# Performance work log

Hardware: AMD Instinct MI355X
Metric: run time of the kernel (lower is better)

## Reference

```python
import jax, jax.numpy as jnp
import numpy as np

LEAKY_ALPHA = 0.2  # tf.nn.leaky_relu default

B, S, E = 16, 4096, 768
H, A = 4, 128  # segments_amount (heads), attention_dimension


def setup_inputs() -> dict:
    key = jax.random.key(0)
    k0, k1, k2 = jax.random.split(key, 3)
    x = jax.random.normal(k0, (B, S, E), dtype=jnp.float32)
    # Per-head MLP params, Glorot-ish scaling
    W1 = jax.random.normal(k1, (H, E, A), dtype=jnp.float32) * (1.0 / np.sqrt(E))
    b1 = jnp.zeros((H, A), dtype=jnp.float32)
    W2 = jax.random.normal(k2, (H, A, E), dtype=jnp.float32) * (1.0 / np.sqrt(A))
    b2 = jnp.zeros((H, E), dtype=jnp.float32)
    return {"x": x, "W1": W1, "b1": b1, "W2": W2, "b2": b2}


def reference(x, W1, b1, W2, b2):
    # Batched over heads h: Dense->LeakyReLU->Dense
    h = jnp.einsum('bse,hea->bhsa', x, W1) + b1[None, :, None, :]
    h = jnp.where(h >= 0, h, LEAKY_ALPHA * h)
    logits = jnp.einsum('bhsa,hae->bhse', h, W2) + b2[None, :, None, :]
    # Softmax over sequence axis (axis=1 in original per-head [B,S,E])
    weights = jax.nn.softmax(logits, axis=2)  # [B,H,S,E]
    # Attention-weighted sum over sequence -> [B,H,E]
    segment_embeddings = jnp.einsum('bse,bhse->bhe', x, weights)
    return segment_embeddings
```

## Files before the change

### kernel.cpp

```cpp
#include <hip/hip_runtime.h>
#include <hip/hip_bf16.h>

#define B_ 16
#define S_ 4096
#define E_ 768
#define H_ 4
#define A_ 128

constexpr float ALPHA = 0.2f;
constexpr float LOG2E = 1.44269504088896340736f;

typedef __attribute__((ext_vector_type(4))) float f32x4;
typedef __attribute__((ext_vector_type(8))) short bf16x8;

__device__ __forceinline__ unsigned short f2bf(float f) {
    union { float f; unsigned int u; } v;
    v.f = f;
    unsigned int u = v.u;
    unsigned int r = (u + 0x7FFFu + ((u >> 16) & 1u)) >> 16;
    return (unsigned short)r;
}

__device__ __forceinline__ unsigned int pk2bf(float lo, float hi) {
    __hip_bfloat162 h2 = __float22bfloat162_rn(make_float2(lo, hi));
    union { __hip_bfloat162 h; unsigned int u; } c;
    c.h = h2;
    return c.u;
}

__global__ __launch_bounds__(256) void k_prep1(const float* __restrict__ w1,
                                               unsigned short* __restrict__ w1t) {
    __shared__ unsigned short t[64 * 65];
    int bid = blockIdx.x;
    int ta = bid & 1;
    int te = (bid >> 1) % 12;
    int h  = bid / 24;
    const float* src = w1 + (size_t)h * E_ * A_;
    unsigned short* dst = w1t + (size_t)h * A_ * E_;
    int tid = threadIdx.x;
#pragma unroll
    for (int it = 0; it < 16; ++it) {
        int idx = it * 256 + tid;
        int r = idx >> 6, c = idx & 63;
        t[r * 65 + c] = f2bf(src[(size_t)(te * 64 + r) * A_ + ta * 64 + c]);
    }
    __syncthreads();
#pragma unroll
    for (int it = 0; it < 16; ++it) {
        int idx = it * 256 + tid;
        int a = idx >> 6, e = idx & 63;
        dst[(size_t)(ta * 64 + a) * E_ + te * 64 + e] = t[e * 65 + a];
    }
}

__global__ __launch_bounds__(256) void k_prep2(const float* __restrict__ w2,
                                               unsigned short* __restrict__ w2t) {
    __shared__ unsigned short t[64 * 65];
    int bid = blockIdx.x;
    int te = bid % 12;
    int ta = (bid / 12) & 1;
    int h  = bid / 24;
    const float* src = w2 + (size_t)h * A_ * E_;
    unsigned short* dst = w2t + (size_t)h * E_ * A_;
    int tid = threadIdx.x;
#pragma unroll
    for (int it = 0; it < 16; ++it) {
        int idx = it * 256 + tid;
        int r = idx >> 6, c = idx & 63;
        t[r * 65 + c] = f2bf(src[(size_t)(ta * 64 + r) * E_ + te * 64 + c] * LOG2E);
    }
    __syncthreads();
#pragma unroll
    for (int it = 0; it < 16; ++it) {
        int idx = it * 256 + tid;
        int e = idx >> 6, a = idx & 63;
        dst[(size_t)(te * 64 + e) * A_ + ta * 64 + a] = t[a * 65 + e];
    }
}

__global__ __launch_bounds__(512, 4) void k_stage1(
    const float* __restrict__ x, const unsigned short* __restrict__ w1t,
    const float* __restrict__ b1, unsigned short* __restrict__ hm) {

    int bid = blockIdx.x;
    int wid = (bid & 7) * 256 + (bid >> 3);
    const int h  = wid & 3;
    const int st = (wid >> 2) & 31;
    const int b  = wid >> 7;
    const int s0 = st * 128;

    const int tid = threadIdx.x;
    const int wv = tid >> 6, lane = tid & 63;
    const int lr = lane & 15, lg = lane >> 4;
    const int sw = wv & 1, aw = wv >> 1;

    __shared__ unsigned short bufA[128 * 64];
    __shared__ unsigned short bufB[128 * 64];

    const int ar = tid >> 2;
    const int ac = tid & 3;
    const float* xp = x + ((size_t)b * S_ + s0 + ar) * E_ + ac * 16;
    const unsigned short* wp = w1t + ((size_t)h * A_ + ar) * E_ + ac * 8;

    f32x4 acc[4][2];
#pragma unroll
    for (int i = 0; i < 4; ++i)
#pragma unroll
        for (int j = 0; j < 2; ++j) acc[i][j] = (f32x4)0.0f;

    f32x4 xreg[4];
    bf16x8 wreg[2];
#pragma unroll
    for (int l = 0; l < 4; ++l) xreg[l] = *(const f32x4*)(xp + l * 4);
#pragma unroll
    for (int l = 0; l < 2; ++l) wreg[l] = *(const bf16x8*)(wp + l * 32);

#pragma unroll 1
    for (int ks = 0; ks < 12; ++ks) {
        if (ks) __syncthreads();
#pragma unroll
        for (int l = 0; l < 4; ++l) {
            uint2 p;
            p.x = pk2bf(xreg[l][0], xreg[l][1]);
            p.y = pk2bf(xreg[l][2], xreg[l][3]);
            int byte = (ar * 128 + (ac * 4 + l) * 8) ^ ((ar & 7) << 4);
            *(uint2*)((char*)bufA + byte) = p;
        }
#pragma unroll
        for (int l = 0; l < 2; ++l) {
            int byte = (ar * 128 + (ac + l * 4) * 16) ^ ((ar & 7) << 4);
            *(bf16x8*)((char*)bufB + byte) = wreg[l];
        }
        __syncthreads();
        if (ks < 11) {
            const float* xq = xp + (ks + 1) * 64;
#pragma unroll
            for (int l = 0; l < 4; ++l) xreg[l] = *(const f32x4*)(xq + l * 4);
            const unsigned short* wq = wp + (ks + 1) * 64;
#pragma unroll
            for (int l = 0; l < 2; ++l) wreg[l] = *(const bf16x8*)(wq + l * 32);
        }
#pragma unroll
        for (int kk = 0; kk < 2; ++kk) {
            bf16x8 xf[4], wf[2];
#pragma unroll
            for (int sf = 0; sf < 4; ++sf) {
                int r = sw * 64 + sf * 16 + lr;
                xf[sf] = *(const bf16x8*)((char*)bufA + ((r * 128 + kk * 64 + lg * 16) ^ ((r & 7) << 4)));
            }
#pragma unroll
            for (int nf = 0; nf < 2; ++nf) {
                int r = aw * 32 + nf * 16 + lr;
                wf[nf] = *(const bf16x8*)((char*)bufB + ((r * 128 + kk * 64 + lg * 16) ^ ((r & 7) << 4)));
            }
#pragma unroll
            for (int sf = 0; sf < 4; ++sf)
#pragma unroll
                for (int nf = 0; nf < 2; ++nf)
                    acc[sf][nf] = __builtin_amdgcn_mfma_f32_16x16x32_bf16(
                        wf[nf], xf[sf], acc[sf][nf], 0, 0, 0);
        }
    }

    const size_t hb = ((size_t)(b * H_ + h) * S_ + s0 + sw * 64) * A_ + aw * 32;
#pragma unroll
    for (int nf = 0; nf < 2; ++nf) {
        f32x4 bv = *(const f32x4*)(b1 + h * A_ + aw * 32 + nf * 16 + lg * 4);
#pragma unroll
        for (int sf = 0; sf < 4; ++sf) {
            f32x4 v = acc[sf][nf] + bv;
#pragma unroll
            for (int j = 0; j < 4; ++j) v[j] = v[j] >= 0.0f ? v[j] : ALPHA * v[j];
            uint2 p;
            p.x = pk2bf(v[0], v[1]);
            p.y = pk2bf(v[2], v[3]);
            *(uint2*)(hm + hb + (size_t)(sf * 16 + lr) * A_ + nf * 16 + lg * 4) = p;
        }
    }
}

__global__ __launch_bounds__(256, 4) void k_stage2(
    const float* __restrict__ x, const unsigned short* __restrict__ hm,
    const unsigned short* __restrict__ w2t,
    float* __restrict__ part_z, float* __restrict__ part_o) {

    int bid = blockIdx.x;
    int wid = (bid & 7) * 256 + (bid >> 3);
    const int h  = wid & 3;
    const int sc = (wid >> 2) & 31;
    const int b  = wid >> 7;
    const int s0 = sc * 128;

    const int tid = threadIdx.x;
    const int wv = tid >> 6, lane = tid & 63;
    const int lr = lane & 15, lg = lane >> 4;

    __shared__ unsigned short hmt[128 * 128];

    {
        const unsigned short* hp = hm + ((size_t)(b * H_ + h) * S_ + s0) * A_;
        int r = tid >> 1;
        int c = tid & 1;
#pragma unroll
        for (int l = 0; l < 8; ++l) {
            int ch = c * 8 + l;
            bf16x8 v = *(const bf16x8*)(hp + (size_t)r * A_ + ch * 8);
            int byte = (r * 256 + ch * 16) ^ ((r & 7) << 4);
            *(bf16x8*)((char*)hmt + byte) = v;
        }
    }
    __syncthreads();

    const float* xb = x + ((size_t)b * S_ + s0) * E_;
    const unsigned short* w2h = w2t + (size_t)h * E_ * A_;
    const size_t pbase = (size_t)(b * H_ + h) * E_ * 32 + sc;

#pragma unroll 1
    for (int et = 0; et < 6; ++et) {
        const int e0 = et * 128 + wv * 32;
        bf16x8 w2f[2][4];
#pragma unroll
        for (int nf = 0; nf < 2; ++nf) {
            const unsigned short* q = w2h + (size_t)(e0 + nf * 16 + lr) * A_ + lg * 8;
#pragma unroll
            for (int k4 = 0; k4 < 4; ++k4) w2f[nf][k4] = *(const bf16x8*)(q + k4 * 32);
        }
        f32x4 zz[2], oo[2];
#pragma unroll
        for (int nf = 0; nf < 2; ++nf) { zz[nf] = (f32x4)0.0f; oo[nf] = (f32x4)0.0f; }

#pragma unroll 2
        for (int itr = 0; itr < 8; ++itr) {
            int srow = itr * 16 + lr;
            bf16x8 hf[4];
#pragma unroll
            for (int k4 = 0; k4 < 4; ++k4)
                hf[k4] = *(const bf16x8*)((char*)hmt +
                          ((srow * 256 + (k4 * 32 + lg * 8) * 2) ^ ((srow & 7) << 4)));
            f32x4 lac[2];
            lac[0] = (f32x4)0.0f; lac[1] = (f32x4)0.0f;
#pragma unroll
            for (int k4 = 0; k4 < 4; ++k4) {
                lac[0] = __builtin_amdgcn_mfma_f32_16x16x32_bf16(w2f[0][k4], hf[k4], lac[0], 0, 0, 0);
                lac[1] = __builtin_amdgcn_mfma_f32_16x16x32_bf16(w2f[1][k4], hf[k4], lac[1], 0, 0, 0);
            }
#pragma unroll
            for (int nf = 0; nf < 2; ++nf) {
                const float* xq = xb + (size_t)srow * E_ + e0 + nf * 16 + lg * 4;
                f32x4 xv = *(const f32x4*)xq;
                f32x4 pv;
#pragma unroll
                for (int j = 0; j < 4; ++j) pv[j] = exp2f(lac[nf][j]);
                zz[nf] += pv;
                oo[nf] += pv * xv;
            }
        }
#pragma unroll
        for (int nf = 0; nf < 2; ++nf)
#pragma unroll
            for (int j = 0; j < 4; ++j) {
                float zv = zz[nf][j], ov = oo[nf][j];
#pragma unroll
                for (int msk = 1; msk < 16; msk <<= 1) {
                    zv += __shfl_xor(zv, msk);
                    ov += __shfl_xor(ov, msk);
                }
                if (lr == 0) {
                    int e = e0 + nf * 16 + lg * 4 + j;
                    part_z[pbase + (size_t)e * 32] = zv;
                    part_o[pbase + (size_t)e * 32] = ov;
                }
            }
    }
}

__global__ __launch_bounds__(256) void k_merge(const float* __restrict__ part_z,
                                               const float* __restrict__ part_o,
                                               float* __restrict__ out) {
    int idx = blockIdx.x * 256 + threadIdx.x;
    if (idx >= B_ * H_ * E_) return;
    const float* pz = part_z + (size_t)idx * 32;
    const float* po = part_o + (size_t)idx * 32;
    float z = 0.f, o = 0.f;
#pragma unroll
    for (int q = 0; q < 8; ++q) {
        f32x4 a = *(const f32x4*)(pz + q * 4);
        f32x4 c = *(const f32x4*)(po + q * 4);
        z += (a[0] + a[1]) + (a[2] + a[3]);
        o += (c[0] + c[1]) + (c[2] + c[3]);
    }
    out[idx] = o / z;
}

extern "C" void kernel_launch(void* const* d_in, const int* in_sizes, int n_in,
                              void* d_out, int out_size, void* d_ws, size_t ws_size,
                              hipStream_t stream) {
    const float* x  = (const float*)d_in[0];
    const float* w1 = (const float*)d_in[1];
    const float* b1 = (const float*)d_in[2];
    const float* w2 = (const float*)d_in[3];
    float* out = (float*)d_out;

    char* ws = (char*)d_ws;
    unsigned short* hmw    = (unsigned short*)ws;
    unsigned short* w1t    = (unsigned short*)(ws + 67108864);
    unsigned short* w2t    = (unsigned short*)(ws + 67895296);
    float*          part_z = (float*)(ws + 68681728);
    float*          part_o = (float*)(ws + 74973184);

    k_prep1 <<<dim3(96),   256, 0, stream>>>(w1, w1t);
    k_prep2 <<<dim3(96),   256, 0, stream>>>(w2, w2t);
    k_stage1<<<dim3(2048), 512, 0, stream>>>(x, w1t, b1, hmw);
    k_stage2<<<dim3(2048), 256, 0, stream>>>(x, hmw, w2t, part_z, part_o);
    k_merge <<<dim3(192),  256, 0, stream>>>(part_z, part_o, out);
}
```

Before: 547.1 us.

## Load stage-1 MFMA operands directly from global memory, dropping LDS staging

The stage-1 GEMM no longer stages x and W1 tiles through shared memory with barriers. Each wave now loads its MFMA fragments straight from global memory into registers and converts x to bf16 in-register. Loads are double-buffered by hand across k-steps, and the wave tiling changes from 2x4 to 4x2. This removes LDS writes, LDS reads and __syncthreads. The cost is that data is no longer shared across waves, so global/L2 traffic rises and the loads are less coalesced (16 rows, 32-byte chunks per lane).

```diff
diff --git a/kernel.cpp b/kernel.cpp
--- a/kernel.cpp
+++ b/kernel.cpp
@@ -26,6 +26,15 @@
     union { __hip_bfloat162 h; unsigned int u; } c;
     c.h = h2;
     return c.u;
+}
+
+__device__ __forceinline__ bf16x8 cvt8(const f32x4 a, const f32x4 b) {
+    union { unsigned int u[4]; bf16x8 v; } r;
+    r.u[0] = pk2bf(a[0], a[1]);
+    r.u[1] = pk2bf(a[2], a[3]);
+    r.u[2] = pk2bf(b[0], b[1]);
+    r.u[3] = pk2bf(b[2], b[3]);
+    return r.v;
 }
 
 __global__ __launch_bounds__(256) void k_prep1(const float* __restrict__ w1,
@@ -92,82 +101,64 @@
     const int tid = threadIdx.x;
     const int wv = tid >> 6, lane = tid & 63;
     const int lr = lane & 15, lg = lane >> 4;
-    const int sw = wv & 1, aw = wv >> 1;
-
-    __shared__ unsigned short bufA[128 * 64];
-    __shared__ unsigned short bufB[128 * 64];
-
-    const int ar = tid >> 2;
-    const int ac = tid & 3;
-    const float* xp = x + ((size_t)b * S_ + s0 + ar) * E_ + ac * 16;
-    const unsigned short* wp = w1t + ((size_t)h * A_ + ar) * E_ + ac * 8;
-
-    f32x4 acc[4][2];
-#pragma unroll
-    for (int i = 0; i < 4; ++i)
-#pragma unroll
-        for (int j = 0; j < 2; ++j) acc[i][j] = (f32x4)0.0f;
-
-    f32x4 xreg[4];
-    bf16x8 wreg[2];
-#pragma unroll
-    for (int l = 0; l < 4; ++l) xreg[l] = *(const f32x4*)(xp + l * 4);
-#pragma unroll
-    for (int l = 0; l < 2; ++l) wreg[l] = *(const bf16x8*)(wp + l * 32);
-
+    const int sw = wv & 3;
+    const int aw = wv >> 2;
+
+    const float* xrow = x + ((size_t)b * S_ + s0 + sw * 32 + lr) * E_ + lg * 8;
+    const unsigned short* wrow = w1t + ((size_t)h * A_ + aw * 64 + lr) * E_ + lg * 8;
+
+    f32x4 acc[2][4];
+#pragma unroll
+    for (int i = 0; i < 2; ++i)
+#pragma unroll
+        for (int j = 0; j < 4; ++j) acc[i][j] = (f32x4)0.0f;
+
+    bf16x8 wA[4], wB[4];
+    f32x4  xA[2][2], xB[2][2];
+
+#define S1_LOADS(WB_, XB_, K0_)                                              \
+    {                                                                        \
+        const int k_ = (K0_);                                                \
+        _Pragma("unroll")                                                    \
+        for (int nf = 0; nf < 4; ++nf)                                       \
+            WB_[nf] = *(const bf16x8*)(wrow + nf * 12288 + k_);              \
+        _Pragma("unroll")                                                    \
+        for (int sf = 0; sf < 2; ++sf) {                                     \
+            XB_[sf][0] = *(const f32x4*)(xrow + sf * 12288 + k_);            \
+            XB_[sf][1] = *(const f32x4*)(xrow + sf * 12288 + k_ + 4);        \
+        }                                                                    \
+    }
+
+#define S1_COMPUTE(WB_, XB_)                                                 \
+    {                                                                        \
+        bf16x8 xb0 = cvt8(XB_[0][0], XB_[0][1]);                             \
+        bf16x8 xb1 = cvt8(XB_[1][0], XB_[1][1]);                             \
+        _Pragma("unroll")                                                    \
+        for (int nf = 0; nf < 4; ++nf) {                                     \
+            acc[0][nf] = __builtin_amdgcn_mfma_f32_16x16x32_bf16(            \
+                WB_[nf], xb0, acc[0][nf], 0, 0, 0);                          \
+            acc[1][nf] = __builtin_amdgcn_mfma_f32_16x16x32_bf16(            \
+                WB_[nf], xb1, acc[1][nf], 0, 0, 0);                          \
+        }                                                                    \
+    }
+
+    S1_LOADS(wA, xA, 0)
 #pragma unroll 1
-    for (int ks = 0; ks < 12; ++ks) {
-        if (ks) __syncthreads();
-#pragma unroll
-        for (int l = 0; l < 4; ++l) {
-            uint2 p;
-            p.x = pk2bf(xreg[l][0], xreg[l][1]);
-            p.y = pk2bf(xreg[l][2], xreg[l][3]);
-            int byte = (ar * 128 + (ac * 4 + l) * 8) ^ ((ar & 7) << 4);
-            *(uint2*)((char*)bufA + byte) = p;
-        }
-#pragma unroll
-        for (int l = 0; l < 2; ++l) {
-            int byte = (ar * 128 + (ac + l * 4) * 16) ^ ((ar & 7) << 4);
-            *(bf16x8*)((char*)bufB + byte) = wreg[l];
-        }
-        __syncthreads();
-        if (ks < 11) {
-            const float* xq = xp + (ks + 1) * 64;
-#pragma unroll
-            for (int l = 0; l < 4; ++l) xreg[l] = *(const f32x4*)(xq + l * 4);
-            const unsigned short* wq = wp + (ks + 1) * 64;
-#pragma unroll
-            for (int l = 0; l < 2; ++l) wreg[l] = *(const bf16x8*)(wq + l * 32);
-        }
-#pragma unroll
-        for (int kk = 0; kk < 2; ++kk) {
-            bf16x8 xf[4], wf[2];
-#pragma unroll
-            for (int sf = 0; sf < 4; ++sf) {
-                int r = sw * 64 + sf * 16 + lr;
-                xf[sf] = *(const bf16x8*)((char*)bufA + ((r * 128 + kk * 64 + lg * 16) ^ ((r & 7) << 4)));
-            }
-#pragma unroll
-            for (int nf = 0; nf < 2; ++nf) {
-                int r = aw * 32 + nf * 16 + lr;
-                wf[nf] = *(const bf16x8*)((char*)bufB + ((r * 128 + kk * 64 + lg * 16) ^ ((r & 7) << 4)));
-            }
-#pragma unroll
-            for (int sf = 0; sf < 4; ++sf)
-#pragma unroll
-                for (int nf = 0; nf < 2; ++nf)
-                    acc[sf][nf] = __builtin_amdgcn_mfma_f32_16x16x32_bf16(
-                        wf[nf], xf[sf], acc[sf][nf], 0, 0, 0);
-        }
-    }
-
-    const size_t hb = ((size_t)(b * H_ + h) * S_ + s0 + sw * 64) * A_ + aw * 32;
-#pragma unroll
-    for (int nf = 0; nf < 2; ++nf) {
-        f32x4 bv = *(const f32x4*)(b1 + h * A_ + aw * 32 + nf * 16 + lg * 4);
-#pragma unroll
-        for (int sf = 0; sf < 4; ++sf) {
+    for (int ks = 0; ks < 24; ks += 2) {
+        if (ks + 1 < 24) S1_LOADS(wB, xB, (ks + 1) * 32)
+        S1_COMPUTE(wA, xA)
+        if (ks + 2 < 24) S1_LOADS(wA, xA, (ks + 2) * 32)
+        S1_COMPUTE(wB, xB)
+    }
+#undef S1_LOADS
+#undef S1_COMPUTE
+
+    const size_t hb = ((size_t)(b * H_ + h) * S_ + s0 + sw * 32) * A_ + aw * 64;
+#pragma unroll
+    for (int nf = 0; nf < 4; ++nf) {
+        f32x4 bv = *(const f32x4*)(b1 + h * A_ + aw * 64 + nf * 16 + lg * 4);
+#pragma unroll
+        for (int sf = 0; sf < 2; ++sf) {
             f32x4 v = acc[sf][nf] + bv;
 #pragma unroll
             for (int j = 0; j < 4; ++j) v[j] = v[j] >= 0.0f ? v[j] : ALPHA * v[j];
```

New measurement: 742.9 us. 35.8% more time.
